# Kernel tuning notes

Measured on AMD Instinct MI355X. Metric: run time of the kernel, lower is better.

Reference implementation:

```python
import jax, jax.numpy as jnp
import numpy as np

EPS = 1e-7  # K.epsilon()
ROUTINGS = 3

def squash(v, axis=-1):
    s2 = jnp.sum(jnp.square(v), axis=axis, keepdims=True)
    scale = s2 / (1.0 + s2) / jnp.sqrt(s2 + EPS)
    return scale * v

def setup_inputs() -> dict:
    key = jax.random.key(0)
    k1, k2 = jax.random.split(key)
    B, IN_CAPS, IN_DIM = 256, 1152, 8
    NUM_CAPS, DIM = 10, 16
    x = jax.random.normal(k1, (B, IN_CAPS, IN_DIM), dtype=jnp.float32)
    W = jax.random.normal(k2, (IN_CAPS, NUM_CAPS, IN_DIM, DIM), dtype=jnp.float32) * 0.05
    return {"x": x, "W": W}

def reference(x, W):
    # u_hat[b,i,j,d] = sum_k x[b,i,k] * W[i,j,k,d]
    u_hat = jnp.einsum('bik,ijkd->bijd', x, W)  # [B, in_caps, num_caps, dim]
    b = jnp.zeros(u_hat.shape[:-1], dtype=u_hat.dtype)  # [B, in_caps, num_caps]
    v = None
    for i in range(ROUTINGS):
        c = jax.nn.softmax(b, axis=2)                       # over num_caps
        s = jnp.einsum('bij,bijd->bjd', c, u_hat)           # [B, num_caps, dim]
        v = squash(s)
        if i < ROUTINGS - 1:
            b = b + jnp.einsum('bijd,bjd->bij', u_hat, v)   # agreement
    return v
```

## Files before the change

### kernel.cpp

```cpp
#include <hip/hip_runtime.h>
#include <cstddef>

#define B_TOT   256
#define IN_CAPS 1152
#define KDIM    8
#define NJ      10
#define ND      16
#define JD      160

#define BB      4
#define ISPLIT  4
#define CI      32
#define IPAR    16
#define NTHREADS 640
#define IRANGE  (IN_CAPS/ISPLIT)
#define NCHUNK  (IRANGE/CI)

__device__ __forceinline__ float dot4(float4 a, float4 b) {
    return a.x*b.x + a.y*b.y + a.z*b.z + a.w*b.w;
}

template<bool FIRST>
__global__ __launch_bounds__(NTHREADS)
void iter_kernel(const float* __restrict__ x, const float* __restrict__ Wt,
                 const float* __restrict__ vsum, float* __restrict__ s_out)
{
    const int g   = blockIdx.x >> 2;
    const int isp = blockIdx.x & 3;
    const int b0  = g * BB;
    const int i_begin = isp * IRANGE;

    const int t = threadIdx.x;
    const int i_par = t / 40;
    const int r  = t - i_par * 40;
    const int j  = r >> 2;
    const int dq = r & 3;

    __shared__ float x_lds[BB][CI][KDIM];
    __shared__ float logit_lds[BB][CI][NJ];
    __shared__ float c_lds[BB][CI][NJ];
    __shared__ float s_lds[BB][JD];

    float4 vs[BB];
    if (!FIRST) {
        #pragma unroll
        for (int bb = 0; bb < BB; ++bb)
            vs[bb] = *(const float4*)(vsum + (size_t)(b0 + bb) * JD + j * ND + dq * 4);
    }

    float4 s_acc[BB];
    #pragma unroll
    for (int bb = 0; bb < BB; ++bb) s_acc[bb] = make_float4(0.f, 0.f, 0.f, 0.f);

    for (int c = 0; c < NCHUNK; ++c) {
        const int ib = i_begin + c * CI;

        if (t < (BB * CI * KDIM) / 4) {
            int bb = t >> 6;
            int f  = t & 63;
            const float4* src = (const float4*)(x + (size_t)(b0 + bb) * IN_CAPS * KDIM
                                                  + (size_t)ib * KDIM);
            ((float4*)&x_lds[bb][0][0])[f] = src[f];
        }
        __syncthreads();

        float4 u[2][BB];
        #pragma unroll
        for (int ii = 0; ii < 2; ++ii) {
            const int i_loc = i_par * 2 + ii;
            const int i = ib + i_loc;
            const float* wrow = Wt + (size_t)(i * NJ + j) * KDIM * ND + dq * 4;
            #pragma unroll
            for (int bb = 0; bb < BB; ++bb) u[ii][bb] = make_float4(0.f, 0.f, 0.f, 0.f);
            #pragma unroll
            for (int k = 0; k < KDIM; ++k) {
                float4 w4 = *(const float4*)(wrow + k * ND);
                #pragma unroll
                for (int bb = 0; bb < BB; ++bb) {
                    float xv = x_lds[bb][i_loc][k];
                    u[ii][bb].x += xv * w4.x;
                    u[ii][bb].y += xv * w4.y;
                    u[ii][bb].z += xv * w4.z;
                    u[ii][bb].w += xv * w4.w;
                }
            }
            if (!FIRST) {
                #pragma unroll
                for (int bb = 0; bb < BB; ++bb) {
                    float lg = dot4(u[ii][bb], vs[bb]);
                    lg += __shfl_xor(lg, 1);
                    lg += __shfl_xor(lg, 2);
                    if (dq == 0) logit_lds[bb][i_loc][j] = lg;
                }
            }
        }

        if (FIRST) {
            #pragma unroll
            for (int ii = 0; ii < 2; ++ii)
                #pragma unroll
                for (int bb = 0; bb < BB; ++bb) {
                    s_acc[bb].x += u[ii][bb].x;
                    s_acc[bb].y += u[ii][bb].y;
                    s_acc[bb].z += u[ii][bb].z;
                    s_acc[bb].w += u[ii][bb].w;
                }
            __syncthreads();
        } else {
            __syncthreads();
            for (int e = t; e < BB * CI * NJ; e += NTHREADS) {
                int bb  = e / (CI * NJ);
                int rem = e - bb * (CI * NJ);
                int il  = rem / NJ;
                int jj  = rem - il * NJ;
                float m = -1e30f;
                #pragma unroll
                for (int q = 0; q < NJ; ++q) m = fmaxf(m, logit_lds[bb][il][q]);
                float ssum = 0.f;
                #pragma unroll
                for (int q = 0; q < NJ; ++q) ssum += __expf(logit_lds[bb][il][q] - m);
                c_lds[bb][il][jj] = __expf(logit_lds[bb][il][jj] - m) / ssum;
            }
            __syncthreads();
            #pragma unroll
            for (int ii = 0; ii < 2; ++ii) {
                const int i_loc = i_par * 2 + ii;
                #pragma unroll
                for (int bb = 0; bb < BB; ++bb) {
                    float cc = c_lds[bb][i_loc][j];
                    s_acc[bb].x += cc * u[ii][bb].x;
                    s_acc[bb].y += cc * u[ii][bb].y;
                    s_acc[bb].z += cc * u[ii][bb].z;
                    s_acc[bb].w += cc * u[ii][bb].w;
                }
            }
        }
    }

    ((float*)s_lds)[t] = 0.f;
    __syncthreads();
    const float premul = FIRST ? 0.1f : 1.0f;
    #pragma unroll
    for (int bb = 0; bb < BB; ++bb) {
        atomicAdd(&s_lds[bb][j * ND + dq * 4 + 0], s_acc[bb].x * premul);
        atomicAdd(&s_lds[bb][j * ND + dq * 4 + 1], s_acc[bb].y * premul);
        atomicAdd(&s_lds[bb][j * ND + dq * 4 + 2], s_acc[bb].z * premul);
        atomicAdd(&s_lds[bb][j * ND + dq * 4 + 3], s_acc[bb].w * premul);
    }
    __syncthreads();
    {
        int bb = t / JD;
        int jd = t - bb * JD;
        unsafeAtomicAdd(&s_out[(size_t)(b0 + bb) * JD + jd], s_lds[bb][jd]);
    }
}

__global__ __launch_bounds__(256)
void squash_kernel(float* __restrict__ s, float* __restrict__ vsum,
                   float* __restrict__ out, int mode)
{
    int idx = blockIdx.x * 256 + threadIdx.x;
    float sv = s[idx];
    float sq = sv * sv;
    sq += __shfl_xor(sq, 1);
    sq += __shfl_xor(sq, 2);
    sq += __shfl_xor(sq, 4);
    sq += __shfl_xor(sq, 8);
    float scale = sq / (1.0f + sq) / sqrtf(sq + 1e-7f);
    float v = sv * scale;
    if (mode == 0) vsum[idx] += v;
    else           out[idx]  = v;
    s[idx] = 0.f;
}

extern "C" void kernel_launch(void* const* d_in, const int* in_sizes, int n_in,
                              void* d_out, int out_size, void* d_ws, size_t ws_size,
                              hipStream_t stream)
{
    const float* x  = (const float*)d_in[0];
    const float* Wt = (const float*)d_in[1];
    float* out  = (float*)d_out;
    float* s    = (float*)d_ws;
    float* vsum = s + (size_t)B_TOT * JD;

    hipMemsetAsync(d_ws, 0, 2 * (size_t)B_TOT * JD * sizeof(float), stream);

    dim3 grid((B_TOT / BB) * ISPLIT), blk(NTHREADS);
    dim3 sgrid((B_TOT * JD) / 256), sblk(256);

    iter_kernel<true><<<grid, blk, 0, stream>>>(x, Wt, nullptr, s);
    squash_kernel<<<sgrid, sblk, 0, stream>>>(s, vsum, out, 0);
    iter_kernel<false><<<grid, blk, 0, stream>>>(x, Wt, vsum, s);
    squash_kernel<<<sgrid, sblk, 0, stream>>>(s, vsum, out, 0);
    iter_kernel<false><<<grid, blk, 0, stream>>>(x, Wt, vsum, s);
    squash_kernel<<<sgrid, sblk, 0, stream>>>(s, vsum, out, 1);
}
```

Before: 197.4 us.

## Fuse squash into routing kernels, preload x slice, and double input-cap split

Each routing pass now recomputes squash of the previous s buffers in its prologue, which removes two of the intermediate squash launches. Separate s buffers per iteration replace the vsum accumulate-and-reset scheme. The block's whole x slice is loaded into LDS once instead of per chunk, and ISPLIT doubles to 8 with CI 16 so each thread handles one input capsule per chunk with W held in registers. This adds more blocks and more global atomics on s, plus some redundant squash work in each block.

```diff
diff --git a/kernel.cpp b/kernel.cpp
--- a/kernel.cpp
+++ b/kernel.cpp
@@ -9,24 +9,27 @@
 #define JD      160
 
 #define BB      4
-#define ISPLIT  4
-#define CI      32
+#define ISPLIT  8
+#define IRANGE  (IN_CAPS/ISPLIT)
+#define CI      16
 #define IPAR    16
 #define NTHREADS 640
-#define IRANGE  (IN_CAPS/ISPLIT)
 #define NCHUNK  (IRANGE/CI)
+#define WSTRIDE (NJ*KDIM*ND)
+#define EPSQ    1e-7f
 
 __device__ __forceinline__ float dot4(float4 a, float4 b) {
     return a.x*b.x + a.y*b.y + a.z*b.z + a.w*b.w;
 }
 
-template<bool FIRST>
-__global__ __launch_bounds__(NTHREADS)
+template<int ITER>
+__global__ __launch_bounds__(NTHREADS, 5)
 void iter_kernel(const float* __restrict__ x, const float* __restrict__ Wt,
-                 const float* __restrict__ vsum, float* __restrict__ s_out)
+                 const float* __restrict__ s1, const float* __restrict__ s2,
+                 float* __restrict__ s_out)
 {
-    const int g   = blockIdx.x >> 2;
-    const int isp = blockIdx.x & 3;
+    const int g   = blockIdx.x >> 3;
+    const int isp = blockIdx.x & 7;
     const int b0  = g * BB;
     const int i_begin = isp * IRANGE;
 
@@ -36,110 +39,126 @@
     const int j  = r >> 2;
     const int dq = r & 3;
 
-    __shared__ float x_lds[BB][CI][KDIM];
+    __shared__ float x_lds[BB][IRANGE][KDIM];
     __shared__ float logit_lds[BB][CI][NJ];
     __shared__ float c_lds[BB][CI][NJ];
     __shared__ float s_lds[BB][JD];
 
     float4 vs[BB];
-    if (!FIRST) {
+    if (ITER >= 2) {
         #pragma unroll
-        for (int bb = 0; bb < BB; ++bb)
-            vs[bb] = *(const float4*)(vsum + (size_t)(b0 + bb) * JD + j * ND + dq * 4);
-    }
+        for (int bb = 0; bb < BB; ++bb) {
+            const float4 a = *(const float4*)(s1 + (size_t)(b0 + bb) * JD + j * ND + dq * 4);
+            float q2 = dot4(a, a);
+            q2 += __shfl_xor(q2, 1);
+            q2 += __shfl_xor(q2, 2);
+            const float sc = q2 / (1.f + q2) / sqrtf(q2 + EPSQ);
+            vs[bb] = make_float4(a.x * sc, a.y * sc, a.z * sc, a.w * sc);
+            if (ITER == 3) {
+                const float4 bv = *(const float4*)(s2 + (size_t)(b0 + bb) * JD + j * ND + dq * 4);
+                float r2 = dot4(bv, bv);
+                r2 += __shfl_xor(r2, 1);
+                r2 += __shfl_xor(r2, 2);
+                const float sc2 = r2 / (1.f + r2) / sqrtf(r2 + EPSQ);
+                vs[bb].x += bv.x * sc2; vs[bb].y += bv.y * sc2;
+                vs[bb].z += bv.z * sc2; vs[bb].w += bv.w * sc2;
+            }
+        }
+    }
+
+    {
+        const int NF = (IRANGE * KDIM) / 4;
+        for (int idx = t; idx < BB * NF; idx += NTHREADS) {
+            const int bb = idx / NF;
+            const int f  = idx - bb * NF;
+            ((float4*)&x_lds[bb][0][0])[f] =
+                ((const float4*)(x + (size_t)(b0 + bb) * IN_CAPS * KDIM
+                                   + (size_t)i_begin * KDIM))[f];
+        }
+    }
+    __syncthreads();
 
     float4 s_acc[BB];
     #pragma unroll
     for (int bb = 0; bb < BB; ++bb) s_acc[bb] = make_float4(0.f, 0.f, 0.f, 0.f);
 
+    const float* wp = Wt + (size_t)((i_begin + i_par) * NJ + j) * (KDIM * ND) + dq * 4;
+
     for (int c = 0; c < NCHUNK; ++c) {
-        const int ib = i_begin + c * CI;
-
-        if (t < (BB * CI * KDIM) / 4) {
-            int bb = t >> 6;
-            int f  = t & 63;
-            const float4* src = (const float4*)(x + (size_t)(b0 + bb) * IN_CAPS * KDIM
-                                                  + (size_t)ib * KDIM);
-            ((float4*)&x_lds[bb][0][0])[f] = src[f];
-        }
-        __syncthreads();
-
-        float4 u[2][BB];
+        float4 w[KDIM];
         #pragma unroll
-        for (int ii = 0; ii < 2; ++ii) {
-            const int i_loc = i_par * 2 + ii;
-            const int i = ib + i_loc;
-            const float* wrow = Wt + (size_t)(i * NJ + j) * KDIM * ND + dq * 4;
-            #pragma unroll
-            for (int bb = 0; bb < BB; ++bb) u[ii][bb] = make_float4(0.f, 0.f, 0.f, 0.f);
+        for (int k = 0; k < KDIM; ++k)
+            w[k] = *(const float4*)(wp + k * ND);
+
+        const int il = c * CI + i_par;
+
+        float4 u[BB];
+        #pragma unroll
+        for (int bb = 0; bb < BB; ++bb) {
+            float xs[KDIM];
+            *(float4*)&xs[0] = *(const float4*)&x_lds[bb][il][0];
+            *(float4*)&xs[4] = *(const float4*)&x_lds[bb][il][4];
+            float4 uu = make_float4(0.f, 0.f, 0.f, 0.f);
             #pragma unroll
             for (int k = 0; k < KDIM; ++k) {
-                float4 w4 = *(const float4*)(wrow + k * ND);
-                #pragma unroll
-                for (int bb = 0; bb < BB; ++bb) {
-                    float xv = x_lds[bb][i_loc][k];
-                    u[ii][bb].x += xv * w4.x;
-                    u[ii][bb].y += xv * w4.y;
-                    u[ii][bb].z += xv * w4.z;
-                    u[ii][bb].w += xv * w4.w;
-                }
-            }
-            if (!FIRST) {
-                #pragma unroll
-                for (int bb = 0; bb < BB; ++bb) {
-                    float lg = dot4(u[ii][bb], vs[bb]);
-                    lg += __shfl_xor(lg, 1);
-                    lg += __shfl_xor(lg, 2);
-                    if (dq == 0) logit_lds[bb][i_loc][j] = lg;
-                }
-            }
-        }
-
-        if (FIRST) {
-            #pragma unroll
-            for (int ii = 0; ii < 2; ++ii)
-                #pragma unroll
-                for (int bb = 0; bb < BB; ++bb) {
-                    s_acc[bb].x += u[ii][bb].x;
-                    s_acc[bb].y += u[ii][bb].y;
-                    s_acc[bb].z += u[ii][bb].z;
-                    s_acc[bb].w += u[ii][bb].w;
-                }
+                uu.x += xs[k] * w[k].x;
+                uu.y += xs[k] * w[k].y;
+                uu.z += xs[k] * w[k].z;
+                uu.w += xs[k] * w[k].w;
+            }
+            u[bb] = uu;
+        }
+
+        if (ITER == 1) {
+            #pragma unroll
+            for (int bb = 0; bb < BB; ++bb) {
+                s_acc[bb].x += u[bb].x; s_acc[bb].y += u[bb].y;
+                s_acc[bb].z += u[bb].z; s_acc[bb].w += u[bb].w;
+            }
+        } else {
+            #pragma unroll
+            for (int bb = 0; bb < BB; ++bb) {
+                float lg = dot4(u[bb], vs[bb]);
+                lg += __shfl_xor(lg, 1);
+                lg += __shfl_xor(lg, 2);
+                if (dq == 0) logit_lds[bb][i_par][j] = lg;
+            }
             __syncthreads();
-        } else {
-            __syncthreads();
-            for (int e = t; e < BB * CI * NJ; e += NTHREADS) {
-                int bb  = e / (CI * NJ);
-                int rem = e - bb * (CI * NJ);
-                int il  = rem / NJ;
-                int jj  = rem - il * NJ;
+
+            {
+                const int bb  = t / (CI * NJ);
+                const int rem = t - bb * (CI * NJ);
+                const int il2 = rem / NJ;
+                const int jj  = rem - il2 * NJ;
+                float lv[NJ];
                 float m = -1e30f;
                 #pragma unroll
-                for (int q = 0; q < NJ; ++q) m = fmaxf(m, logit_lds[bb][il][q]);
-                float ssum = 0.f;
+                for (int q = 0; q < NJ; ++q) { lv[q] = logit_lds[bb][il2][q]; m = fmaxf(m, lv[q]); }
+                float ssum = 0.f, ex = 0.f;
                 #pragma unroll
-                for (int q = 0; q < NJ; ++q) ssum += __expf(logit_lds[bb][il][q] - m);
-                c_lds[bb][il][jj] = __expf(logit_lds[bb][il][jj] - m) / ssum;
+                for (int q = 0; q < NJ; ++q) {
+                    const float e = __expf(lv[q] - m);
+                    ssum += e;
+                    if (q == jj) ex = e;
+                }
+                c_lds[bb][il2][jj] = ex / ssum;
             }
             __syncthreads();
-            #pragma unroll
-            for (int ii = 0; ii < 2; ++ii) {
-                const int i_loc = i_par * 2 + ii;
-                #pragma unroll
-                for (int bb = 0; bb < BB; ++bb) {
-                    float cc = c_lds[bb][i_loc][j];
-                    s_acc[bb].x += cc * u[ii][bb].x;
-                    s_acc[bb].y += cc * u[ii][bb].y;
-                    s_acc[bb].z += cc * u[ii][bb].z;
-                    s_acc[bb].w += cc * u[ii][bb].w;
-                }
-            }
-        }
+
+            #pragma unroll
+            for (int bb = 0; bb < BB; ++bb) {
+                const float cc = c_lds[bb][i_par][j];
+                s_acc[bb].x += cc * u[bb].x; s_acc[bb].y += cc * u[bb].y;
+                s_acc[bb].z += cc * u[bb].z; s_acc[bb].w += cc * u[bb].w;
+            }
+        }
+
+        wp += (size_t)CI * WSTRIDE;
     }
 
     ((float*)s_lds)[t] = 0.f;
     __syncthreads();
-    const float premul = FIRST ? 0.1f : 1.0f;
+    const float premul = (ITER == 1) ? 0.1f : 1.0f;
     #pragma unroll
     for (int bb = 0; bb < BB; ++bb) {
         atomicAdd(&s_lds[bb][j * ND + dq * 4 + 0], s_acc[bb].x * premul);
@@ -149,28 +168,24 @@
     }
     __syncthreads();
     {
-        int bb = t / JD;
-        int jd = t - bb * JD;
+        const int bb = t / JD;
+        const int jd = t - bb * JD;
         unsafeAtomicAdd(&s_out[(size_t)(b0 + bb) * JD + jd], s_lds[bb][jd]);
     }
 }
 
 __global__ __launch_bounds__(256)
-void squash_kernel(float* __restrict__ s, float* __restrict__ vsum,
-                   float* __restrict__ out, int mode)
+void squash_kernel(const float* __restrict__ s, float* __restrict__ out)
 {
-    int idx = blockIdx.x * 256 + threadIdx.x;
-    float sv = s[idx];
+    const int idx = blockIdx.x * 256 + threadIdx.x;
+    const float sv = s[idx];
     float sq = sv * sv;
     sq += __shfl_xor(sq, 1);
     sq += __shfl_xor(sq, 2);
     sq += __shfl_xor(sq, 4);
     sq += __shfl_xor(sq, 8);
-    float scale = sq / (1.0f + sq) / sqrtf(sq + 1e-7f);
-    float v = sv * scale;
-    if (mode == 0) vsum[idx] += v;
-    else           out[idx]  = v;
-    s[idx] = 0.f;
+    const float scale = sq / (1.0f + sq) / sqrtf(sq + EPSQ);
+    out[idx] = sv * scale;
 }
 
 extern "C" void kernel_launch(void* const* d_in, const int* in_sizes, int n_in,
@@ -179,19 +194,17 @@
 {
     const float* x  = (const float*)d_in[0];
     const float* Wt = (const float*)d_in[1];
-    float* out  = (float*)d_out;
-    float* s    = (float*)d_ws;
-    float* vsum = s + (size_t)B_TOT * JD;
-
-    hipMemsetAsync(d_ws, 0, 2 * (size_t)B_TOT * JD * sizeof(float), stream);
+    float* out = (float*)d_out;
+    float* s1  = (float*)d_ws;
+    float* s2  = s1 + (size_t)B_TOT * JD;
+    float* s3  = s2 + (size_t)B_TOT * JD;
+
+    hipMemsetAsync(d_ws, 0, 3 * (size_t)B_TOT * JD * sizeof(float), stream);
 
     dim3 grid((B_TOT / BB) * ISPLIT), blk(NTHREADS);
-    dim3 sgrid((B_TOT * JD) / 256), sblk(256);
-
-    iter_kernel<true><<<grid, blk, 0, stream>>>(x, Wt, nullptr, s);
-    squash_kernel<<<sgrid, sblk, 0, stream>>>(s, vsum, out, 0);
-    iter_kernel<false><<<grid, blk, 0, stream>>>(x, Wt, vsum, s);
-    squash_kernel<<<sgrid, sblk, 0, stream>>>(s, vsum, out, 0);
-    iter_kernel<false><<<grid, blk, 0, stream>>>(x, Wt, vsum, s);
-    squash_kernel<<<sgrid, sblk, 0, stream>>>(s, vsum, out, 1);
-}
+
+    iter_kernel<1><<<grid, blk, 0, stream>>>(x, Wt, nullptr, nullptr, s1);
+    iter_kernel<2><<<grid, blk, 0, stream>>>(x, Wt, s1, nullptr, s2);
+    iter_kernel<3><<<grid, blk, 0, stream>>>(x, Wt, s1, s2, s3);
+    squash_kernel<<<dim3((B_TOT * JD) / 256), dim3(256), 0, stream>>>(s3, out);
+}
```

Measured after the change: 275.1 us. 1.39x slower.
